# Kernel optimization log

Hardware: AMD Instinct MI355X
Metric: run time of the kernel (lower is better)

The kernel has to match this reference:

```python
import jax, jax.numpy as jnp
import numpy as np

H, D, DM, L, B = 16, 64, 1024, 256, 64
SCALE = 1.0 / np.sqrt(D)   # 1/sqrt(d_head)
CHUNK = 64
LN_EPS = 1e-5


def setup_inputs() -> dict:
    key = jax.random.key(0)
    k0, k1, k2, k3 = jax.random.split(key, 4)
    h = jax.random.normal(k0, (L, B, DM), jnp.float32)
    qkv_w = jax.random.normal(k1, (H * 4 * D, DM), jnp.float32) * 0.02
    o_w = jax.random.normal(k2, (DM, H * D), jnp.float32) * 0.02
    ln_gamma = jnp.ones((DM,), jnp.float32)
    ln_beta = jnp.zeros((DM,), jnp.float32)
    pi0 = jax.random.uniform(k3, (H, 256), jnp.float32)
    return {"h": h, "qkv_w": qkv_w, "o_w": o_w,
            "ln_gamma": ln_gamma, "ln_beta": ln_beta, "pi0": pi0}


def _phi(x):
    # elu(x) + 1, then sum-normalize over feature dim
    e = jax.nn.elu(x) + 1.0
    return e / e.sum(-1, keepdims=True)


def _fast_weight_sum(q, k, v):
    # q,k,v: [B,H,L,D]. out[t] = q_t @ W_t, W_t = sum_{s<=t} k_s v_s^T (inclusive).
    # Chunked-recurrent form: intra-chunk causal GEMM + inter-chunk carried state.
    Bb, Hh, Ll, Dd = q.shape
    nc = Ll // CHUNK
    rs = lambda x: x.reshape(Bb, Hh, nc, CHUNK, Dd).transpose(2, 0, 1, 3, 4)  # [nc,B,H,C,D]
    qc, kc, vc = rs(q), rs(k), rs(v)
    mask = jnp.tril(jnp.ones((CHUNK, CHUNK), q.dtype))  # inclusive causal

    def step(W, xs):
        qi, ki, vi = xs  # [B,H,C,D]
        scores = jnp.einsum('bhtd,bhsd->bhts', qi, ki) * mask
        out = jnp.einsum('bhts,bhsd->bhtd', scores, vi) \
            + jnp.einsum('bhtd,bhde->bhte', qi, W)
        W = W + jnp.einsum('bhsd,bhse->bhde', ki, vi)
        return W, out

    W0 = jnp.zeros((Bb, Hh, Dd, Dd), q.dtype)
    _, outs = jax.lax.scan(step, W0, (qc, kc, vc))  # outs: [nc,B,H,C,D]
    return outs.transpose(1, 2, 0, 3, 4).reshape(Bb, Hh, Ll, Dd)


def reference(h, qkv_w, o_w, ln_gamma, ln_beta, pi0):
    slen, bsz, _ = h.shape
    # qkv projection and head split (rbf2keys: q, k1, k2, v)
    qkv = (h @ qkv_w.T).reshape(slen, bsz, H, 4 * D)
    hq, hk1, hk2, hv = jnp.split(qkv, 4, axis=-1)       # each [L,B,H,D]
    perm = lambda x: x.transpose(1, 2, 0, 3)            # -> [B,H,L,D]
    hq, hk1, hk2, hv = perm(hq), perm(hk1), perm(hk2), perm(hv)

    hq = _phi(hq)
    hk1 = _phi(hk1)
    hk2 = _phi(hk2)

    out1 = _fast_weight_sum(hq, hk1, hv)
    out2 = _fast_weight_sum(hq, hk2, hv)

    # skip_attn_normalization=True path: pi0-gated mixture of the two memories
    p = jnp.clip(pi0, 0.0, 1.0)[None, :, :slen, None]   # [1,H,L,1]
    layer_out = SCALE * (out1 * p + out2 * (1.0 - p))   # [B,H,L,D]

    # [B,H,L,D] -> [L,B,H*D]
    layer_out = layer_out.transpose(0, 2, 1, 3).reshape(bsz, slen, H * D).transpose(1, 0, 2)
    attn_out = layer_out @ o_w.T                        # [L,B,DM]

    # post-LN residual (pre_lnorm=False)
    x = h + attn_out
    mu = x.mean(-1, keepdims=True)
    var = ((x - mu) ** 2).mean(-1, keepdims=True)
    return (x - mu) / jnp.sqrt(var + LN_EPS) * ln_gamma + ln_beta
```

## Files before the change

### kernel.cpp

```cpp
#include <hip/hip_runtime.h>
#include <type_traits>


typedef short v8s __attribute__((ext_vector_type(8)));
typedef float v4f __attribute__((ext_vector_type(4)));

__device__ __forceinline__ float bf2f(short s) {
    unsigned int u = ((unsigned int)(unsigned short)s) << 16;
    float f;
    __builtin_memcpy(&f, &u, 4);
    return f;
}
__device__ __forceinline__ short f2bf(float f) {
    unsigned int u;
    __builtin_memcpy(&u, &f, 4);
    u = u + 0x7fffu + ((u >> 16) & 1u);
    return (short)(u >> 16);
}

__device__ __forceinline__ void load_lds16(const short* g, short* l) {
    __builtin_amdgcn_global_load_lds((const __attribute__((address_space(1))) void*)g,
                                     (__attribute__((address_space(3))) void*)l, 16, 0, 0);
}

__global__ void __launch_bounds__(256)
cvt_bf16(const float* __restrict__ in, short* __restrict__ out, int n4) {
    int i = blockIdx.x * 256 + threadIdx.x;
    if (i >= n4) return;
    float4 v = ((const float4*)in)[i];
    short4 o;
    o.x = f2bf(v.x); o.y = f2bf(v.y); o.z = f2bf(v.z); o.w = f2bf(v.w);
    ((short4*)out)[i] = o;
}

template <typename OutT>
__global__ void __launch_bounds__(512, 2)
gemm_nt(const short* __restrict__ Ap, const short* __restrict__ Bp,
        OutT* __restrict__ C, int M, int N, int K) {
    __shared__ __align__(16) short lds[2][2][256 * 64];

    const int tid = threadIdx.x;
    const int w = tid >> 6, lane = tid & 63;
    const int wm = w >> 2, wn = w & 3;
    const int lq = lane >> 4, lr = lane & 15;
    const int asw = (lr & 7) * 8;
    const int rr = tid >> 3;
    const int scol = ((tid & 7) * 8) ^ ((rr & 7) * 8);

    int bid = blockIdx.y * gridDim.x + blockIdx.x;
    int nwg = gridDim.x * gridDim.y;
    int swz = (bid & 7) * (nwg >> 3) + (bid >> 3);
    int bm = swz % gridDim.x, bn = swz / gridDim.x;

    v4f acc[8][4] = {};
    v8s a[4][2];
    v8s b[2][2][2];

    const int NT = K >> 6;
    const int nIter = NT >> 1;

#define BAR_() do { asm volatile("" ::: "memory"); __builtin_amdgcn_s_barrier(); asm volatile("" ::: "memory"); } while (0)
#define VMCNT4_() asm volatile("s_waitcnt vmcnt(4)" ::: "memory")
#define STAGE_(MAT, BUF, HALF, KT) do { \
        const short* g_ = ((MAT) ? Bp : Ap) + \
            (long)(((MAT) ? bn : bm) * 256 + (HALF) * 128 + rr) * K + (KT) * 64 + scol; \
        short* l_ = &lds[BUF][MAT][(HALF) * 8192] + w * 512; \
        load_lds16(g_, l_); \
        load_lds16(g_ + (long)64 * K, l_ + 4096); \
    } while (0)
#define LDA_(QM, BUF) do { \
        _Pragma("unroll") \
        for (int mi = 0; mi < 4; ++mi) { \
            const short* pa_ = &lds[BUF][0][(wm * 128 + (QM) * 64 + mi * 16 + lr) * 64]; \
            a[mi][0] = *(const v8s*)&pa_[(lq * 8) ^ asw]; \
            a[mi][1] = *(const v8s*)&pa_[(32 + lq * 8) ^ asw]; \
        } \
    } while (0)
#define LDB_(QN, BUF) do { \
        _Pragma("unroll") \
        for (int ni = 0; ni < 2; ++ni) { \
            const short* pb_ = &lds[BUF][1][(wn * 64 + (QN) * 32 + ni * 16 + lr) * 64]; \
            b[QN][ni][0] = *(const v8s*)&pb_[(lq * 8) ^ asw]; \
            b[QN][ni][1] = *(const v8s*)&pb_[(32 + lq * 8) ^ asw]; \
        } \
    } while (0)
#define MFMA_(QM, QN) do { \
        __builtin_amdgcn_s_setprio(1); \
        _Pragma("unroll") \
        for (int kk = 0; kk < 2; ++kk) \
            _Pragma("unroll") \
            for (int mi = 0; mi < 4; ++mi) \
                _Pragma("unroll") \
                for (int ni = 0; ni < 2; ++ni) \
                    acc[(QM) * 4 + mi][(QN) * 2 + ni] = __builtin_amdgcn_mfma_f32_16x16x32_bf16( \
                        a[mi][kk], b[QN][ni][kk], acc[(QM) * 4 + mi][(QN) * 2 + ni], 0, 0, 0); \
        __builtin_amdgcn_s_setprio(0); \
    } while (0)

    STAGE_(1, 0, 0, 0);
    STAGE_(1, 0, 1, 0);
    STAGE_(0, 0, 0, 0);
    STAGE_(0, 0, 1, 0);
    STAGE_(1, 1, 0, 1);
    STAGE_(1, 1, 1, 1);
    VMCNT4_();
    BAR_();

    for (int it = 0; it < nIter; ++it) {
        const int t = 2 * it;
        const int t1 = t + 1;
        int t2 = t + 2; if (t2 >= NT) t2 -= NT;
        int t3 = t + 3; if (t3 >= NT) t3 -= NT;

        LDA_(0, 0); LDB_(0, 0);
        STAGE_(0, 1, 0, t1);
        BAR_(); MFMA_(0, 0); BAR_();
        LDB_(1, 0);
        STAGE_(0, 1, 1, t1);
        BAR_(); MFMA_(0, 1); BAR_();
        LDA_(1, 0);
        STAGE_(1, 0, 0, t2);
        BAR_(); MFMA_(1, 0); BAR_();
        STAGE_(1, 0, 1, t2);
        VMCNT4_();
        BAR_(); MFMA_(1, 1); BAR_();
        LDA_(0, 1); LDB_(0, 1);
        STAGE_(0, 0, 0, t2);
        BAR_(); MFMA_(0, 0); BAR_();
        LDB_(1, 1);
        STAGE_(0, 0, 1, t2);
        BAR_(); MFMA_(0, 1); BAR_();
        LDA_(1, 1);
        STAGE_(1, 1, 0, t3);
        BAR_(); MFMA_(1, 0); BAR_();
        STAGE_(1, 1, 1, t3);
        VMCNT4_();
        BAR_(); MFMA_(1, 1); BAR_();
    }

#undef BAR_
#undef VMCNT4_
#undef STAGE_
#undef LDA_
#undef LDB_
#undef MFMA_

#pragma unroll
    for (int m = 0; m < 8; ++m)
#pragma unroll
        for (int n = 0; n < 4; ++n)
#pragma unroll
            for (int r = 0; r < 4; ++r) {
                int row = bm * 256 + wm * 128 + m * 16 + lq * 4 + r;
                int col = bn * 256 + wn * 64 + n * 16 + lr;
                float v = acc[m][n][r];
                if constexpr (std::is_same_v<OutT, short>)
                    C[(long)row * N + col] = f2bf(v);
                else
                    C[(long)row * N + col] = v;
            }
}

#define SW(row, s) ((row) * 72 + ((((s) >> 3) ^ (((row) >> 4) & 7)) << 3) + ((s) & 7))

__global__ void __launch_bounds__(256)
fastweight(const short* __restrict__ qkv, short* __restrict__ out1, short* __restrict__ out2) {
    const int bid = blockIdx.x;
    const int mem = bid & 1, h = (bid >> 1) & 15, b = bid >> 5;
    const int tid = threadIdx.x;
    const int w = tid >> 6, lane = tid & 63;
    const int lq = lane >> 4, lr = lane & 15;
    __shared__ __align__(16) short sq[64 * 72];
    __shared__ __align__(16) short skS[64 * 72];
    __shared__ __align__(16) short skT[64 * 72];
    __shared__ __align__(16) short svT[64 * 72];
    __shared__ __align__(16) short sWT[64 * 72];
    short* outbuf = mem ? out2 : out1;
    const int koff = 64 + mem * 64;

    for (int i = tid; i < 64 * 36; i += 256) ((int*)sWT)[i] = 0;

    const int r = tid >> 2, seg = (tid & 3) * 16;

    v4f wacc[4] = {};

    for (int c = 0; c < 4; c++) {
        __syncthreads();
        const long gbase = ((long)((c * 64 + r) * 64 + b)) * 4096 + h * 256;
        {
            union { int4 v[2]; short s[16]; } u;
            u.v[0] = *(const int4*)(qkv + gbase + seg);
            u.v[1] = *(const int4*)(qkv + gbase + seg + 8);
            float f[16]; float ssum = 0.f;
#pragma unroll
            for (int i = 0; i < 16; i++) {
                float x = bf2f(u.s[i]);
                float e = x > 0.f ? x + 1.f : __expf(x);
                f[i] = e; ssum += e;
            }
            ssum += __shfl_xor(ssum, 1, 64);
            ssum += __shfl_xor(ssum, 2, 64);
            float inv = 1.f / ssum;
            union { int4 v[2]; short s[16]; } o;
#pragma unroll
            for (int i = 0; i < 16; i++) o.s[i] = f2bf(f[i] * inv);
            *(int4*)&sq[SW(r, seg)] = o.v[0];
            *(int4*)&sq[SW(r, seg + 8)] = o.v[1];
        }
        {
            union { int4 v[2]; short s[16]; } u;
            u.v[0] = *(const int4*)(qkv + gbase + koff + seg);
            u.v[1] = *(const int4*)(qkv + gbase + koff + seg + 8);
            float f[16]; float ssum = 0.f;
#pragma unroll
            for (int i = 0; i < 16; i++) {
                float x = bf2f(u.s[i]);
                float e = x > 0.f ? x + 1.f : __expf(x);
                f[i] = e; ssum += e;
            }
            ssum += __shfl_xor(ssum, 1, 64);
            ssum += __shfl_xor(ssum, 2, 64);
            float inv = 1.f / ssum;
            union { int4 v[2]; short s[16]; } o;
#pragma unroll
            for (int i = 0; i < 16; i++) o.s[i] = f2bf(f[i] * inv);
            *(int4*)&skS[SW(r, seg)] = o.v[0];
            *(int4*)&skS[SW(r, seg + 8)] = o.v[1];
#pragma unroll
            for (int i = 0; i < 16; i++) skT[SW(seg + i, r)] = o.s[i];
        }
        {
            union { int4 v[2]; short s[16]; } u;
            u.v[0] = *(const int4*)(qkv + gbase + 192 + seg);
            u.v[1] = *(const int4*)(qkv + gbase + 192 + seg + 8);
#pragma unroll
            for (int i = 0; i < 16; i++) svT[SW(seg + i, r)] = u.s[i];
        }
        __syncthreads();

        v8s qa0 = *(const v8s*)&sq[SW(16 * w + lr, lq * 8)];
        v8s qa1 = *(const v8s*)&sq[SW(16 * w + lr, 32 + lq * 8)];

        v4f sacc[4];
#pragma unroll
        for (int n = 0; n < 4; n++) {
            v8s b0 = *(const v8s*)&skS[SW(16 * n + lr, lq * 8)];
            v8s b1 = *(const v8s*)&skS[SW(16 * n + lr, 32 + lq * 8)];
            v4f t = {};
            t = __builtin_amdgcn_mfma_f32_16x16x32_bf16(qa0, b0, t, 0, 0, 0);
            t = __builtin_amdgcn_mfma_f32_16x16x32_bf16(qa1, b1, t, 0, 0, 0);
            sacc[n] = t;
        }
        __syncthreads();
#pragma unroll
        for (int n = 0; n < 4; n++)
#pragma unroll
            for (int rr = 0; rr < 4; rr++) {
                int t_ = 16 * w + lq * 4 + rr;
                int s_ = 16 * n + lr;
                skS[SW(t_, s_)] = f2bf(s_ <= t_ ? sacc[n][rr] : 0.f);
            }

        v8s sa0 = *(const v8s*)&skS[SW(16 * w + lr, lq * 8)];
        v8s sa1 = *(const v8s*)&skS[SW(16 * w + lr, 32 + lq * 8)];
        v4f oacc[4];
#pragma unroll
        for (int n = 0; n < 4; n++) {
            v8s vb0 = *(const v8s*)&svT[SW(16 * n + lr, lq * 8)];
            v8s vb1 = *(const v8s*)&svT[SW(16 * n + lr, 32 + lq * 8)];
            v8s wb0 = *(const v8s*)&sWT[SW(16 * n + lr, lq * 8)];
            v8s wb1 = *(const v8s*)&sWT[SW(16 * n + lr, 32 + lq * 8)];
            v4f t = {};
            t = __builtin_amdgcn_mfma_f32_16x16x32_bf16(sa0, vb0, t, 0, 0, 0);
            t = __builtin_amdgcn_mfma_f32_16x16x32_bf16(sa1, vb1, t, 0, 0, 0);
            t = __builtin_amdgcn_mfma_f32_16x16x32_bf16(qa0, wb0, t, 0, 0, 0);
            t = __builtin_amdgcn_mfma_f32_16x16x32_bf16(qa1, wb1, t, 0, 0, 0);
            oacc[n] = t;
        }
#pragma unroll
        for (int n = 0; n < 4; n++)
#pragma unroll
            for (int rr = 0; rr < 4; rr++) {
                int t_ = 16 * w + lq * 4 + rr;
                long o = ((long)((c * 64 + t_) * 64 + b)) * 1024 + h * 64 + 16 * n + lr;
                outbuf[o] = f2bf(oacc[n][rr]);
            }

        if (c < 3) {
            __syncthreads();
            v8s va0 = *(const v8s*)&svT[SW(16 * w + lr, lq * 8)];
            v8s va1 = *(const v8s*)&svT[SW(16 * w + lr, 32 + lq * 8)];
#pragma unroll
            for (int n = 0; n < 4; n++) {
                v8s kb0 = *(const v8s*)&skT[SW(16 * n + lr, lq * 8)];
                v8s kb1 = *(const v8s*)&skT[SW(16 * n + lr, 32 + lq * 8)];
                wacc[n] = __builtin_amdgcn_mfma_f32_16x16x32_bf16(va0, kb0, wacc[n], 0, 0, 0);
                wacc[n] = __builtin_amdgcn_mfma_f32_16x16x32_bf16(va1, kb1, wacc[n], 0, 0, 0);
            }
#pragma unroll
            for (int n = 0; n < 4; n++)
#pragma unroll
                for (int rr = 0; rr < 4; rr++)
                    sWT[SW(16 * w + lq * 4 + rr, 16 * n + lr)] = f2bf(wacc[n][rr]);
        }
    }
}

__global__ void __launch_bounds__(256)
mix_kernel(const short* __restrict__ l1, const short* __restrict__ l2,
           const float* __restrict__ pi0, short* __restrict__ outm) {
    long idx8 = ((long)blockIdx.x * 256 + threadIdx.x) * 8;
    int col = (int)(idx8 & 1023);
    int row = (int)(idx8 >> 10);
    int hh = col >> 6;
    int l = row >> 6;
    float p = pi0[hh * 256 + l];
    p = fminf(fmaxf(p, 0.f), 1.f);
    float q = 1.f - p;
    union { int4 v; short s[8]; } ua, ub, uo;
    ua.v = *(const int4*)(l1 + idx8);
    ub.v = *(const int4*)(l2 + idx8);
#pragma unroll
    for (int i = 0; i < 8; i++)
        uo.s[i] = f2bf(0.125f * (p * bf2f(ua.s[i]) + q * bf2f(ub.s[i])));
    *(int4*)(outm + idx8) = uo.v;
}

__global__ void __launch_bounds__(256)
ln_kernel(const float* __restrict__ h, const float* __restrict__ attn,
          const float* __restrict__ gamma, const float* __restrict__ beta,
          float* __restrict__ out) {
    const int row = blockIdx.x;
    const long base = (long)row * 1024;
    const int tid = threadIdx.x;
    float4 xh = ((const float4*)(h + base))[tid];
    float4 xa = ((const float4*)(attn + base))[tid];
    float4 x;
    x.x = xh.x + xa.x; x.y = xh.y + xa.y; x.z = xh.z + xa.z; x.w = xh.w + xa.w;
    float s = x.x + x.y + x.z + x.w;
    float s2 = x.x * x.x + x.y * x.y + x.z * x.z + x.w * x.w;
#pragma unroll
    for (int m = 32; m > 0; m >>= 1) {
        s += __shfl_xor(s, m, 64);
        s2 += __shfl_xor(s2, m, 64);
    }
    __shared__ float ps[4], ps2[4];
    int w = tid >> 6, lane = tid & 63;
    if (lane == 0) { ps[w] = s; ps2[w] = s2; }
    __syncthreads();
    s = ps[0] + ps[1] + ps[2] + ps[3];
    s2 = ps2[0] + ps2[1] + ps2[2] + ps2[3];
    float mu = s * (1.f / 1024.f);
    float var = s2 * (1.f / 1024.f) - mu * mu;
    float inv = rsqrtf(var + 1e-5f);
    float4 g = ((const float4*)gamma)[tid];
    float4 bb = ((const float4*)beta)[tid];
    float4 o;
    o.x = (x.x - mu) * inv * g.x + bb.x;
    o.y = (x.y - mu) * inv * g.y + bb.y;
    o.z = (x.z - mu) * inv * g.z + bb.z;
    o.w = (x.w - mu) * inv * g.w + bb.w;
    ((float4*)(out + base))[tid] = o;
}

extern "C" void kernel_launch(void* const* d_in, const int* in_sizes, int n_in,
                              void* d_out, int out_size, void* d_ws, size_t ws_size,
                              hipStream_t stream) {
    const float* h     = (const float*)d_in[0];
    const float* qkvw  = (const float*)d_in[1];
    const float* ow    = (const float*)d_in[2];
    const float* gamma = (const float*)d_in[3];
    const float* beta  = (const float*)d_in[4];
    const float* pi0   = (const float*)d_in[5];
    float* out = (float*)d_out;
    char* ws = (char*)d_ws;

    short* h_bf   = (short*)(ws);
    short* wq_bf  = (short*)(ws + 33554432);
    short* wo_bf  = (short*)(ws + 41943040);
    short* qkv_bf = (short*)(ws + 44040192);
    short* l1     = (short*)(ws + 178257920);
    short* l2     = (short*)(ws + 211812352);
    float* attnf  = (float*)(ws + 44040192);
    short* lmix   = h_bf;

    cvt_bf16<<<16384, 256, 0, stream>>>(h, h_bf, 16777216 / 4);
    cvt_bf16<<<4096, 256, 0, stream>>>(qkvw, wq_bf, 4194304 / 4);
    cvt_bf16<<<1024, 256, 0, stream>>>(ow, wo_bf, 1048576 / 4);

    gemm_nt<short><<<dim3(64, 16), 512, 0, stream>>>(h_bf, wq_bf, qkv_bf, 16384, 4096, 1024);

    fastweight<<<2048, 256, 0, stream>>>(qkv_bf, l1, l2);

    mix_kernel<<<8192, 256, 0, stream>>>(l1, l2, pi0, lmix);

    gemm_nt<float><<<dim3(64, 4), 512, 0, stream>>>(lmix, wo_bf, attnf, 16384, 1024, 1024);

    ln_kernel<<<16384, 256, 0, stream>>>(h, attnf, gamma, beta, out);
}
```

Baseline: 415.9 us.

## Fuse both fast-weight memories and pi0 mixing into one kernel; reschedule GEMM barriers

The fastweight kernel now handles both key memories for one (batch, head) in a single block. It shares the q and v loads and the phi(q) computation, and applies the pi0-gated mix directly in its epilogue. This removes the separate mix kernel along with the l1/l2 intermediate buffers and their global traffic. The block count halves and LDS use per block roughly doubles, which may lower occupancy. Separately, the GEMM main loop hoists the B-fragment LDS loads, removes barriers before each MFMA group and adds sched_barrier hints, trading synchronization for a possible LDS hazard risk.

```diff
diff --git a/kernel.cpp b/kernel.cpp
--- a/kernel.cpp
+++ b/kernel.cpp
@@ -60,6 +60,7 @@
     const int nIter = NT >> 1;
 
 #define BAR_() do { asm volatile("" ::: "memory"); __builtin_amdgcn_s_barrier(); asm volatile("" ::: "memory"); } while (0)
+#define SBAR_() __builtin_amdgcn_sched_barrier(0)
 #define VMCNT4_() asm volatile("s_waitcnt vmcnt(4)" ::: "memory")
 #define STAGE_(MAT, BUF, HALF, KT) do { \
         const short* g_ = ((MAT) ? Bp : Ap) + \
@@ -107,38 +108,46 @@
     BAR_();
 
     for (int it = 0; it < nIter; ++it) {
-        const int t = 2 * it;
-        const int t1 = t + 1;
-        int t2 = t + 2; if (t2 >= NT) t2 -= NT;
-        int t3 = t + 3; if (t3 >= NT) t3 -= NT;
-
-        LDA_(0, 0); LDB_(0, 0);
+        const int t1 = 2 * it + 1;
+        int t2 = 2 * it + 2; if (t2 >= NT) t2 -= NT;
+        int t3 = 2 * it + 3; if (t3 >= NT) t3 -= NT;
+
+        LDA_(0, 0); LDB_(0, 0); LDB_(1, 0);
         STAGE_(0, 1, 0, t1);
-        BAR_(); MFMA_(0, 0); BAR_();
-        LDB_(1, 0);
+        MFMA_(0, 0);
+        SBAR_(); BAR_();
         STAGE_(0, 1, 1, t1);
-        BAR_(); MFMA_(0, 1); BAR_();
+        MFMA_(0, 1);
+        SBAR_();
         LDA_(1, 0);
+        SBAR_(); BAR_();
         STAGE_(1, 0, 0, t2);
-        BAR_(); MFMA_(1, 0); BAR_();
+        MFMA_(1, 0);
+        SBAR_(); BAR_();
         STAGE_(1, 0, 1, t2);
         VMCNT4_();
-        BAR_(); MFMA_(1, 1); BAR_();
-        LDA_(0, 1); LDB_(0, 1);
+        MFMA_(1, 1);
+        SBAR_(); BAR_();
+        LDA_(0, 1); LDB_(0, 1); LDB_(1, 1);
         STAGE_(0, 0, 0, t2);
-        BAR_(); MFMA_(0, 0); BAR_();
-        LDB_(1, 1);
+        MFMA_(0, 0);
+        SBAR_(); BAR_();
         STAGE_(0, 0, 1, t2);
-        BAR_(); MFMA_(0, 1); BAR_();
+        MFMA_(0, 1);
+        SBAR_();
         LDA_(1, 1);
+        SBAR_(); BAR_();
         STAGE_(1, 1, 0, t3);
-        BAR_(); MFMA_(1, 0); BAR_();
+        MFMA_(1, 0);
+        SBAR_(); BAR_();
         STAGE_(1, 1, 1, t3);
         VMCNT4_();
-        BAR_(); MFMA_(1, 1); BAR_();
+        MFMA_(1, 1);
+        SBAR_(); BAR_();
     }
 
 #undef BAR_
+#undef SBAR_
 #undef VMCNT4_
 #undef STAGE_
 #undef LDA_
@@ -163,72 +172,63 @@
 
 #define SW(row, s) ((row) * 72 + ((((s) >> 3) ^ (((row) >> 4) & 7)) << 3) + ((s) & 7))
 
+__device__ __forceinline__ void phi_store(const short* __restrict__ g,
+                                          short* sS, short* sT, int r, int seg) {
+    union { int4 v[2]; short s[16]; } u;
+    u.v[0] = *(const int4*)(g);
+    u.v[1] = *(const int4*)(g + 8);
+    float f[16]; float ssum = 0.f;
+#pragma unroll
+    for (int i = 0; i < 16; i++) {
+        float x = bf2f(u.s[i]);
+        float e = x > 0.f ? x + 1.f : __expf(x);
+        f[i] = e; ssum += e;
+    }
+    ssum += __shfl_xor(ssum, 1, 64);
+    ssum += __shfl_xor(ssum, 2, 64);
+    float inv = 1.f / ssum;
+    union { int4 v[2]; short s[16]; } o;
+#pragma unroll
+    for (int i = 0; i < 16; i++) o.s[i] = f2bf(f[i] * inv);
+    *(int4*)&sS[SW(r, seg)] = o.v[0];
+    *(int4*)&sS[SW(r, seg + 8)] = o.v[1];
+    if (sT) {
+#pragma unroll
+        for (int i = 0; i < 16; i++) sT[SW(seg + i, r)] = o.s[i];
+    }
+}
+
 __global__ void __launch_bounds__(256)
-fastweight(const short* __restrict__ qkv, short* __restrict__ out1, short* __restrict__ out2) {
+fastweight(const short* __restrict__ qkv, const float* __restrict__ pi0,
+           short* __restrict__ outm) {
     const int bid = blockIdx.x;
-    const int mem = bid & 1, h = (bid >> 1) & 15, b = bid >> 5;
+    const int h = bid & 15, b = bid >> 4;
     const int tid = threadIdx.x;
     const int w = tid >> 6, lane = tid & 63;
     const int lq = lane >> 4, lr = lane & 15;
     __shared__ __align__(16) short sq[64 * 72];
-    __shared__ __align__(16) short skS[64 * 72];
-    __shared__ __align__(16) short skT[64 * 72];
+    __shared__ __align__(16) short sk1S[64 * 72];
+    __shared__ __align__(16) short sk2S[64 * 72];
+    __shared__ __align__(16) short sk1T[64 * 72];
+    __shared__ __align__(16) short sk2T[64 * 72];
     __shared__ __align__(16) short svT[64 * 72];
-    __shared__ __align__(16) short sWT[64 * 72];
-    short* outbuf = mem ? out2 : out1;
-    const int koff = 64 + mem * 64;
-
-    for (int i = tid; i < 64 * 36; i += 256) ((int*)sWT)[i] = 0;
+    __shared__ __align__(16) short sW1T[64 * 72];
+    __shared__ __align__(16) short sW2T[64 * 72];
+    __shared__ float spi[256];
+
+    for (int i = tid; i < 64 * 36; i += 256) { ((int*)sW1T)[i] = 0; ((int*)sW2T)[i] = 0; }
+    spi[tid] = pi0[h * 256 + tid];
 
     const int r = tid >> 2, seg = (tid & 3) * 16;
 
-    v4f wacc[4] = {};
+    v4f wacc1[4] = {}, wacc2[4] = {};
 
     for (int c = 0; c < 4; c++) {
         __syncthreads();
         const long gbase = ((long)((c * 64 + r) * 64 + b)) * 4096 + h * 256;
-        {
-            union { int4 v[2]; short s[16]; } u;
-            u.v[0] = *(const int4*)(qkv + gbase + seg);
-            u.v[1] = *(const int4*)(qkv + gbase + seg + 8);
-            float f[16]; float ssum = 0.f;
-#pragma unroll
-            for (int i = 0; i < 16; i++) {
-                float x = bf2f(u.s[i]);
-                float e = x > 0.f ? x + 1.f : __expf(x);
-                f[i] = e; ssum += e;
-            }
-            ssum += __shfl_xor(ssum, 1, 64);
-            ssum += __shfl_xor(ssum, 2, 64);
-            float inv = 1.f / ssum;
-            union { int4 v[2]; short s[16]; } o;
-#pragma unroll
-            for (int i = 0; i < 16; i++) o.s[i] = f2bf(f[i] * inv);
-            *(int4*)&sq[SW(r, seg)] = o.v[0];
-            *(int4*)&sq[SW(r, seg + 8)] = o.v[1];
-        }
-        {
-            union { int4 v[2]; short s[16]; } u;
-            u.v[0] = *(const int4*)(qkv + gbase + koff + seg);
-            u.v[1] = *(const int4*)(qkv + gbase + koff + seg + 8);
-            float f[16]; float ssum = 0.f;
-#pragma unroll
-            for (int i = 0; i < 16; i++) {
-                float x = bf2f(u.s[i]);
-                float e = x > 0.f ? x + 1.f : __expf(x);
-                f[i] = e; ssum += e;
-            }
-            ssum += __shfl_xor(ssum, 1, 64);
-            ssum += __shfl_xor(ssum, 2, 64);
-            float inv = 1.f / ssum;
-            union { int4 v[2]; short s[16]; } o;
-#pragma unroll
-            for (int i = 0; i < 16; i++) o.s[i] = f2bf(f[i] * inv);
-            *(int4*)&skS[SW(r, seg)] = o.v[0];
-            *(int4*)&skS[SW(r, seg + 8)] = o.v[1];
-#pragma unroll
-            for (int i = 0; i < 16; i++) skT[SW(seg + i, r)] = o.s[i];
-        }
+        phi_store(qkv + gbase + seg, sq, nullptr, r, seg);
+        phi_store(qkv + gbase + 64 + seg, sk1S, sk1T, r, seg);
+        phi_store(qkv + gbase + 128 + seg, sk2S, sk2T, r, seg);
         {
             union { int4 v[2]; short s[16]; } u;
             u.v[0] = *(const int4*)(qkv + gbase + 192 + seg);
@@ -241,15 +241,19 @@
         v8s qa0 = *(const v8s*)&sq[SW(16 * w + lr, lq * 8)];
         v8s qa1 = *(const v8s*)&sq[SW(16 * w + lr, 32 + lq * 8)];
 
-        v4f sacc[4];
+        v4f sacc1[4], sacc2[4];
 #pragma unroll
         for (int n = 0; n < 4; n++) {
-            v8s b0 = *(const v8s*)&skS[SW(16 * n + lr, lq * 8)];
-            v8s b1 = *(const v8s*)&skS[SW(16 * n + lr, 32 + lq * 8)];
-            v4f t = {};
-            t = __builtin_amdgcn_mfma_f32_16x16x32_bf16(qa0, b0, t, 0, 0, 0);
-            t = __builtin_amdgcn_mfma_f32_16x16x32_bf16(qa1, b1, t, 0, 0, 0);
-            sacc[n] = t;
+            v8s b10 = *(const v8s*)&sk1S[SW(16 * n + lr, lq * 8)];
+            v8s b11 = *(const v8s*)&sk1S[SW(16 * n + lr, 32 + lq * 8)];
+            v8s b20 = *(const v8s*)&sk2S[SW(16 * n + lr, lq * 8)];
+            v8s b21 = *(const v8s*)&sk2S[SW(16 * n + lr, 32 + lq * 8)];
+            v4f t1 = {}, t2 = {};
+            t1 = __builtin_amdgcn_mfma_f32_16x16x32_bf16(qa0, b10, t1, 0, 0, 0);
+            t2 = __builtin_amdgcn_mfma_f32_16x16x32_bf16(qa0, b20, t2, 0, 0, 0);
+            t1 = __builtin_amdgcn_mfma_f32_16x16x32_bf16(qa1, b11, t1, 0, 0, 0);
+            t2 = __builtin_amdgcn_mfma_f32_16x16x32_bf16(qa1, b21, t2, 0, 0, 0);
+            sacc1[n] = t1; sacc2[n] = t2;
         }
         __syncthreads();
 #pragma unroll
@@ -258,32 +262,44 @@
             for (int rr = 0; rr < 4; rr++) {
                 int t_ = 16 * w + lq * 4 + rr;
                 int s_ = 16 * n + lr;
-                skS[SW(t_, s_)] = f2bf(s_ <= t_ ? sacc[n][rr] : 0.f);
+                sk1S[SW(t_, s_)] = f2bf(s_ <= t_ ? sacc1[n][rr] : 0.f);
+                sk2S[SW(t_, s_)] = f2bf(s_ <= t_ ? sacc2[n][rr] : 0.f);
             }
 
-        v8s sa0 = *(const v8s*)&skS[SW(16 * w + lr, lq * 8)];
-        v8s sa1 = *(const v8s*)&skS[SW(16 * w + lr, 32 + lq * 8)];
-        v4f oacc[4];
+        v8s sa10 = *(const v8s*)&sk1S[SW(16 * w + lr, lq * 8)];
+        v8s sa11 = *(const v8s*)&sk1S[SW(16 * w + lr, 32 + lq * 8)];
+        v8s sa20 = *(const v8s*)&sk2S[SW(16 * w + lr, lq * 8)];
+        v8s sa21 = *(const v8s*)&sk2S[SW(16 * w + lr, 32 + lq * 8)];
+        v4f o1[4], o2[4];
 #pragma unroll
         for (int n = 0; n < 4; n++) {
             v8s vb0 = *(const v8s*)&svT[SW(16 * n + lr, lq * 8)];
             v8s vb1 = *(const v8s*)&svT[SW(16 * n + lr, 32 + lq * 8)];
-            v8s wb0 = *(const v8s*)&sWT[SW(16 * n + lr, lq * 8)];
-            v8s wb1 = *(const v8s*)&sWT[SW(16 * n + lr, 32 + lq * 8)];
-            v4f t = {};
-            t = __builtin_amdgcn_mfma_f32_16x16x32_bf16(sa0, vb0, t, 0, 0, 0);
-            t = __builtin_amdgcn_mfma_f32_16x16x32_bf16(sa1, vb1, t, 0, 0, 0);
-            t = __builtin_amdgcn_mfma_f32_16x16x32_bf16(qa0, wb0, t, 0, 0, 0);
-            t = __builtin_amdgcn_mfma_f32_16x16x32_bf16(qa1, wb1, t, 0, 0, 0);
-            oacc[n] = t;
+            v8s wb10 = *(const v8s*)&sW1T[SW(16 * n + lr, lq * 8)];
+            v8s wb11 = *(const v8s*)&sW1T[SW(16 * n + lr, 32 + lq * 8)];
+            v8s wb20 = *(const v8s*)&sW2T[SW(16 * n + lr, lq * 8)];
+            v8s wb21 = *(const v8s*)&sW2T[SW(16 * n + lr, 32 + lq * 8)];
+            v4f t1 = {}, t2 = {};
+            t1 = __builtin_amdgcn_mfma_f32_16x16x32_bf16(sa10, vb0, t1, 0, 0, 0);
+            t2 = __builtin_amdgcn_mfma_f32_16x16x32_bf16(sa20, vb0, t2, 0, 0, 0);
+            t1 = __builtin_amdgcn_mfma_f32_16x16x32_bf16(sa11, vb1, t1, 0, 0, 0);
+            t2 = __builtin_amdgcn_mfma_f32_16x16x32_bf16(sa21, vb1, t2, 0, 0, 0);
+            t1 = __builtin_amdgcn_mfma_f32_16x16x32_bf16(qa0, wb10, t1, 0, 0, 0);
+            t2 = __builtin_amdgcn_mfma_f32_16x16x32_bf16(qa0, wb20, t2, 0, 0, 0);
+            t1 = __builtin_amdgcn_mfma_f32_16x16x32_bf16(qa1, wb11, t1, 0, 0, 0);
+            t2 = __builtin_amdgcn_mfma_f32_16x16x32_bf16(qa1, wb21, t2, 0, 0, 0);
+            o1[n] = t1; o2[n] = t2;
         }
 #pragma unroll
         for (int n = 0; n < 4; n++)
 #pragma unroll
             for (int rr = 0; rr < 4; rr++) {
                 int t_ = 16 * w + lq * 4 + rr;
-                long o = ((long)((c * 64 + t_) * 64 + b)) * 1024 + h * 64 + 16 * n + lr;
-                outbuf[o] = f2bf(oacc[n][rr]);
+                int l = c * 64 + t_;
+                float p = fminf(fmaxf(spi[l], 0.f), 1.f);
+                float val = 0.125f * (p * o1[n][rr] + (1.f - p) * o2[n][rr]);
+                long o = ((long)(l * 64 + b)) * 1024 + h * 64 + 16 * n + lr;
+                outm[o] = f2bf(val);
             }
 
         if (c < 3) {
@@ -292,38 +308,24 @@
             v8s va1 = *(const v8s*)&svT[SW(16 * w + lr, 32 + lq * 8)];
 #pragma unroll
             for (int n = 0; n < 4; n++) {
-                v8s kb0 = *(const v8s*)&skT[SW(16 * n + lr, lq * 8)];
-                v8s kb1 = *(const v8s*)&skT[SW(16 * n + lr, 32 + lq * 8)];
-                wacc[n] = __builtin_amdgcn_mfma_f32_16x16x32_bf16(va0, kb0, wacc[n], 0, 0, 0);
-                wacc[n] = __builtin_amdgcn_mfma_f32_16x16x32_bf16(va1, kb1, wacc[n], 0, 0, 0);
+                v8s kb10 = *(const v8s*)&sk1T[SW(16 * n + lr, lq * 8)];
+                v8s kb11 = *(const v8s*)&sk1T[SW(16 * n + lr, 32 + lq * 8)];
+                v8s kb20 = *(const v8s*)&sk2T[SW(16 * n + lr, lq * 8)];
+                v8s kb21 = *(const v8s*)&sk2T[SW(16 * n + lr, 32 + lq * 8)];
+                wacc1[n] = __builtin_amdgcn_mfma_f32_16x16x32_bf16(va0, kb10, wacc1[n], 0, 0, 0);
+                wacc2[n] = __builtin_amdgcn_mfma_f32_16x16x32_bf16(va0, kb20, wacc2[n], 0, 0, 0);
+                wacc1[n] = __builtin_amdgcn_mfma_f32_16x16x32_bf16(va1, kb11, wacc1[n], 0, 0, 0);
+                wacc2[n] = __builtin_amdgcn_mfma_f32_16x16x32_bf16(va1, kb21, wacc2[n], 0, 0, 0);
             }
 #pragma unroll
             for (int n = 0; n < 4; n++)
 #pragma unroll
-                for (int rr = 0; rr < 4; rr++)
-                    sWT[SW(16 * w + lq * 4 + rr, 16 * n + lr)] = f2bf(wacc[n][rr]);
+                for (int rr = 0; rr < 4; rr++) {
+                    sW1T[SW(16 * w + lq * 4 + rr, 16 * n + lr)] = f2bf(wacc1[n][rr]);
+                    sW2T[SW(16 * w + lq * 4 + rr, 16 * n + lr)] = f2bf(wacc2[n][rr]);
+                }
         }
     }
-}
-
-__global__ void __launch_bounds__(256)
-mix_kernel(const short* __restrict__ l1, const short* __restrict__ l2,
-           const float* __restrict__ pi0, short* __restrict__ outm) {
-    long idx8 = ((long)blockIdx.x * 256 + threadIdx.x) * 8;
-    int col = (int)(idx8 & 1023);
-    int row = (int)(idx8 >> 10);
-    int hh = col >> 6;
-    int l = row >> 6;
-    float p = pi0[hh * 256 + l];
-    p = fminf(fmaxf(p, 0.f), 1.f);
-    float q = 1.f - p;
-    union { int4 v; short s[8]; } ua, ub, uo;
-    ua.v = *(const int4*)(l1 + idx8);
-    ub.v = *(const int4*)(l2 + idx8);
-#pragma unroll
-    for (int i = 0; i < 8; i++)
-        uo.s[i] = f2bf(0.125f * (p * bf2f(ua.s[i]) + q * bf2f(ub.s[i])));
-    *(int4*)(outm + idx8) = uo.v;
 }
 
 __global__ void __launch_bounds__(256)
@@ -379,8 +381,6 @@
     short* wq_bf  = (short*)(ws + 33554432);
     short* wo_bf  = (short*)(ws + 41943040);
     short* qkv_bf = (short*)(ws + 44040192);
-    short* l1     = (short*)(ws + 178257920);
-    short* l2     = (short*)(ws + 211812352);
     float* attnf  = (float*)(ws + 44040192);
     short* lmix   = h_bf;
 
@@ -390,9 +390,7 @@
 
     gemm_nt<short><<<dim3(64, 16), 512, 0, stream>>>(h_bf, wq_bf, qkv_bf, 16384, 4096, 1024);
 
-    fastweight<<<2048, 256, 0, stream>>>(qkv_bf, l1, l2);
-
-    mix_kernel<<<8192, 256, 0, stream>>>(l1, l2, pi0, lmix);
+    fastweight<<<1024, 256, 0, stream>>>(qkv_bf, pi0, lmix);
 
     gemm_nt<float><<<dim3(64, 4), 512, 0, stream>>>(lmix, wo_bf, attnf, 16384, 1024, 1024);
 
```

After: 419.4 us. About the same (+0.9%).
